# Kernel tuning notes

Hardware: AMD Instinct MI355X
Metric: run time of the kernel (lower is better)

## Reference

```python
import jax, jax.numpy as jnp
import numpy as np

N, E, D = 20000, 640000, 64
NEG_SLOPE = 0.2

def setup_inputs() -> dict:
    key = jax.random.key(0)
    ks = jax.random.split(key, 8)
    x = jax.random.normal(ks[0], (N, D), dtype=jnp.float32)
    edge_index = jax.random.randint(ks[1], (2, E), 0, N, dtype=jnp.int64)
    w0 = jax.random.normal(ks[2], (N, D, D), dtype=jnp.float32) * 0.1
    att0 = jax.random.normal(ks[3], (N, 2 * D, 1), dtype=jnp.float32) * 0.1
    b0 = jax.random.normal(ks[4], (D,), dtype=jnp.float32) * 0.1
    w1 = jax.random.normal(ks[5], (N, D, D), dtype=jnp.float32) * 0.1
    att1 = jax.random.normal(ks[6], (N, 2 * D, 1), dtype=jnp.float32) * 0.1
    b1 = jax.random.normal(ks[7], (D,), dtype=jnp.float32) * 0.1
    return {"x": x, "edge_index": edge_index, "w0": w0, "att0": att0,
            "b0": b0, "w1": w1, "att1": att1, "b1": b1}

def _gat_layer(x, row, col, w, att_w, b):
    n = x.shape[0]
    # per-node dynamic weight bmm: [N,1,D] @ [N,D,D] -> [N,D]
    h = jnp.einsum('nd,nde->ne', x, w)
    h_i = h[row]                      # source messages [E, D]
    h_j = h[col]                      # destination features [E, D]
    att_in = jnp.concatenate([h_i, h_j], axis=1)      # [E, 2D]
    a = att_w[row][:, :, 0]                            # [E, 2D]
    scores = jnp.einsum('ed,ed->e', att_in, a)         # [E]
    scores = jnp.where(scores >= 0, scores, NEG_SLOPE * scores)  # leaky_relu(0.2)
    # segment softmax over destination node (col), replaces python loop over unique(col)
    seg_max = jax.ops.segment_max(scores, col, num_segments=n)
    ex = jnp.exp(scores - seg_max[col])
    seg_sum = jax.ops.segment_sum(ex, col, num_segments=n)
    att = ex / seg_sum[col]
    out = jax.ops.segment_sum(h_i * att[:, None], col, num_segments=n)
    return out + b

def reference(x, edge_index, w0, att0, b0, w1, att1, b1):
    row, col = edge_index[0], edge_index[1]
    h = _gat_layer(x, row, col, w0, att0, b0)
    h = jax.nn.relu(h)  # inter-layer activation; dropout inactive in eval mode
    out = _gat_layer(h, row, col, w1, att1, b1)
    return out
```

## Files before the change

### kernel.cpp

```cpp
#include <hip/hip_runtime.h>
#include <hip/hip_bf16.h>

#define NN 20000
#define EE 640000
#define DD 64


__global__ void zero_kernel(int* __restrict__ p, int n) {
    int i = blockIdx.x * blockDim.x + threadIdx.x;
    if (i < n) p[i] = 0;
}

__global__ void hist_kernel(const int* __restrict__ col, int* __restrict__ counts) {
    int e = blockIdx.x * blockDim.x + threadIdx.x;
    if (e < EE) {
        int c = col[e];
        if ((unsigned)c >= NN) c = 0;
        atomicAdd(&counts[c], 1);
    }
}

__global__ void scan_kernel(const int* __restrict__ counts, int* __restrict__ offsets) {
    const int T = 1024;
    const int per = (NN + T - 1) / T;
    int tid = threadIdx.x;
    int start = tid * per;
    int s = 0;
    for (int i = 0; i < per; ++i) { int idx = start + i; if (idx < NN) s += counts[idx]; }
    __shared__ int sm[T];
    sm[tid] = s;
    __syncthreads();
    for (int off = 1; off < T; off <<= 1) {
        int t = (tid >= off) ? sm[tid - off] : 0;
        __syncthreads();
        sm[tid] += t;
        __syncthreads();
    }
    int run = sm[tid] - s;
    for (int i = 0; i < per; ++i) {
        int idx = start + i;
        if (idx < NN) { offsets[idx] = run; run += counts[idx]; }
    }
    if (tid == T - 1) offsets[NN] = sm[T - 1];
}

__global__ void scatter_kernel(const int* __restrict__ row, const int* __restrict__ col,
                               const int* __restrict__ offsets, int* __restrict__ cursor,
                               int* __restrict__ srcs) {
    int e = blockIdx.x * blockDim.x + threadIdx.x;
    if (e < EE) {
        int c = col[e];
        if ((unsigned)c >= NN) c = 0;
        int r = row[e];
        if ((unsigned)r >= NN) r = 0;
        int p = atomicAdd(&cursor[c], 1);
        srcs[offsets[c] + p] = r;
    }
}


__global__ __launch_bounds__(256) void node_h_kernel(
    const float* __restrict__ x,
    const float* __restrict__ w,
    const float* __restrict__ att,
    float* __restrict__ hs,
    float* __restrict__ s1)
{
    int wave = (blockIdx.x * blockDim.x + threadIdx.x) >> 6;
    int lane = threadIdx.x & 63;
    if (wave >= NN) return;
    int n = wave;

    float xval = x[(size_t)n * 64 + lane];

    int eg = lane & 15;
    int dg = lane >> 4;
    float acc[4] = {0.f, 0.f, 0.f, 0.f};

    const float* wbase = w + (size_t)n * 4096;
    #pragma unroll
    for (int it = 0; it < 16; ++it) {
        int d = it * 4 + dg;
        float xv = __shfl(xval, d, 64);
        float4 r = *(const float4*)(wbase + d * 64 + eg * 4);
        acc[0] += xv * r.x;
        acc[1] += xv * r.y;
        acc[2] += xv * r.z;
        acc[3] += xv * r.w;
    }
    #pragma unroll
    for (int j = 0; j < 4; ++j) {
        acc[j] += __shfl_xor(acc[j], 16, 64);
        acc[j] += __shfl_xor(acc[j], 32, 64);
    }
    if (dg == 0) {
        *(float4*)(hs + (size_t)n * 128 + eg * 4) = make_float4(acc[0], acc[1], acc[2], acc[3]);
    }
    hs[(size_t)n * 128 + 64 + lane] = att[(size_t)n * 128 + 64 + lane];

    float4 a = *(const float4*)(att + (size_t)n * 128 + eg * 4);
    float p = acc[0] * a.x + acc[1] * a.y + acc[2] * a.z + acc[3] * a.w;
    p += __shfl_xor(p, 1, 64);
    p += __shfl_xor(p, 2, 64);
    p += __shfl_xor(p, 4, 64);
    p += __shfl_xor(p, 8, 64);
    if (lane == 0) s1[n] = p;
}


template<bool LAYER0>
__global__ __launch_bounds__(256) void edge_aggr_kernel(
    const float* __restrict__ hs,
    const float* __restrict__ s1,
    const float* __restrict__ bias,
    const int* __restrict__ offsets,
    const int* __restrict__ srcs,
    float* __restrict__ out)
{
    int wave = (blockIdx.x * blockDim.x + threadIdx.x) >> 6;
    int lane = threadIdx.x & 63;
    if (wave >= NN) return;
    int c = wave;

    float hc = hs[(size_t)c * 128 + lane];
    int beg = offsets[c];
    int end = offsets[c + 1];

    float sum0 = 0.f, sum1 = 0.f, sum2 = 0.f, sum3 = 0.f;
    float acc0 = 0.f, acc1 = 0.f, acc2 = 0.f, acc3 = 0.f;

    int i = beg;
    for (; i + 4 <= end; i += 4) {
        int r0 = srcs[i + 0]; if ((unsigned)r0 >= NN) r0 = 0;
        int r1 = srcs[i + 1]; if ((unsigned)r1 >= NN) r1 = 0;
        int r2 = srcs[i + 2]; if ((unsigned)r2 >= NN) r2 = 0;
        int r3 = srcs[i + 3]; if ((unsigned)r3 >= NN) r3 = 0;
        const float* b0p = hs + (size_t)r0 * 128;
        const float* b1p = hs + (size_t)r1 * 128;
        const float* b2p = hs + (size_t)r2 * 128;
        const float* b3p = hs + (size_t)r3 * 128;
        float a20 = b0p[64 + lane];
        float a21 = b1p[64 + lane];
        float a22 = b2p[64 + lane];
        float a23 = b3p[64 + lane];
        float h0 = b0p[lane];
        float h1 = b1p[lane];
        float h2 = b2p[lane];
        float h3 = b3p[lane];
        float s10 = s1[r0], s11 = s1[r1], s12 = s1[r2], s13 = s1[r3];

        float p0 = hc * a20, p1 = hc * a21, p2 = hc * a22, p3 = hc * a23;
        #pragma unroll
        for (int s = 1; s < 64; s <<= 1) {
            p0 += __shfl_xor(p0, s, 64);
            p1 += __shfl_xor(p1, s, 64);
            p2 += __shfl_xor(p2, s, 64);
            p3 += __shfl_xor(p3, s, 64);
        }
        float sc0 = p0 + s10; sc0 = (sc0 >= 0.f) ? sc0 : 0.2f * sc0;
        float sc1 = p1 + s11; sc1 = (sc1 >= 0.f) ? sc1 : 0.2f * sc1;
        float sc2 = p2 + s12; sc2 = (sc2 >= 0.f) ? sc2 : 0.2f * sc2;
        float sc3 = p3 + s13; sc3 = (sc3 >= 0.f) ? sc3 : 0.2f * sc3;
        float e0 = __expf(sc0), e1 = __expf(sc1), e2 = __expf(sc2), e3 = __expf(sc3);
        sum0 += e0; sum1 += e1; sum2 += e2; sum3 += e3;
        acc0 = fmaf(e0, h0, acc0);
        acc1 = fmaf(e1, h1, acc1);
        acc2 = fmaf(e2, h2, acc2);
        acc3 = fmaf(e3, h3, acc3);
    }
    for (; i < end; ++i) {
        int r = srcs[i]; if ((unsigned)r >= NN) r = 0;
        const float* bp = hs + (size_t)r * 128;
        float a2 = bp[64 + lane];
        float hr = bp[lane];
        float p = hc * a2;
        #pragma unroll
        for (int s = 1; s < 64; s <<= 1) p += __shfl_xor(p, s, 64);
        float sc = p + s1[r];
        sc = (sc >= 0.f) ? sc : 0.2f * sc;
        float e = __expf(sc);
        sum0 += e;
        acc0 = fmaf(e, hr, acc0);
    }

    float sum = (sum0 + sum1) + (sum2 + sum3);
    float acc = (acc0 + acc1) + (acc2 + acc3);

    float b = bias[lane];
    float o = (end > beg) ? (acc / sum + b) : b;
    if (LAYER0) o = fmaxf(o, 0.f);
    out[(size_t)c * 64 + lane] = o;
}


extern "C" void kernel_launch(void* const* d_in, const int* in_sizes, int n_in,
                              void* d_out, int out_size, void* d_ws, size_t ws_size,
                              hipStream_t stream) {
    const float* x    = (const float*)d_in[0];
    const int*   ei   = (const int*)d_in[1];
    const float* w0   = (const float*)d_in[2];
    const float* att0 = (const float*)d_in[3];
    const float* b0   = (const float*)d_in[4];
    const float* w1   = (const float*)d_in[5];
    const float* att1 = (const float*)d_in[6];
    const float* b1   = (const float*)d_in[7];

    const int* row = ei;
    const int* col = ei + EE;

    char* base = (char*)d_ws;
    float* hs      = (float*)(base);
    float* xmid    = (float*)(base + 10240000);
    float* s1      = (float*)(base + 15360000);
    int*   counts  = (int*)(base + 15440000);
    int*   cursor  = (int*)(base + 15520000);
    int*   offsets = (int*)(base + 15600000);
    int*   srcs    = (int*)(base + 15680016);

    zero_kernel<<<(2 * NN + 255) / 256, 256, 0, stream>>>(counts, 2 * NN);
    hist_kernel<<<(EE + 255) / 256, 256, 0, stream>>>(col, counts);
    scan_kernel<<<1, 1024, 0, stream>>>(counts, offsets);
    scatter_kernel<<<(EE + 255) / 256, 256, 0, stream>>>(row, col, offsets, cursor, srcs);

    const int hblocks = (NN + 3) / 4;

    node_h_kernel<<<hblocks, 256, 0, stream>>>(x, w0, att0, hs, s1);
    edge_aggr_kernel<true><<<hblocks, 256, 0, stream>>>(hs, s1, b0, offsets, srcs, xmid);
    node_h_kernel<<<hblocks, 256, 0, stream>>>(xmid, w1, att1, hs, s1);
    edge_aggr_kernel<false><<<hblocks, 256, 0, stream>>>(hs, s1, b1, offsets, srcs,
                                                         (float*)d_out);
}
```

Measured before the change: 833.3 us.

## Split wave into four 16-lane groups processing edges with float4 loads

Result: faster. 800.5 us (-3.9%).

```diff
diff --git a/kernel.cpp b/kernel.cpp
--- a/kernel.cpp
+++ b/kernel.cpp
@@ -121,75 +121,95 @@
     int lane = threadIdx.x & 63;
     if (wave >= NN) return;
     int c = wave;
-
-    float hc = hs[(size_t)c * 128 + lane];
+    int g = lane >> 4;
+    int q = lane & 15;
+
+    float4 hcv = *(const float4*)(hs + (size_t)c * 128 + q * 4);
     int beg = offsets[c];
     int end = offsets[c + 1];
 
-    float sum0 = 0.f, sum1 = 0.f, sum2 = 0.f, sum3 = 0.f;
-    float acc0 = 0.f, acc1 = 0.f, acc2 = 0.f, acc3 = 0.f;
-
-    int i = beg;
-    for (; i + 4 <= end; i += 4) {
-        int r0 = srcs[i + 0]; if ((unsigned)r0 >= NN) r0 = 0;
-        int r1 = srcs[i + 1]; if ((unsigned)r1 >= NN) r1 = 0;
-        int r2 = srcs[i + 2]; if ((unsigned)r2 >= NN) r2 = 0;
-        int r3 = srcs[i + 3]; if ((unsigned)r3 >= NN) r3 = 0;
-        const float* b0p = hs + (size_t)r0 * 128;
-        const float* b1p = hs + (size_t)r1 * 128;
-        const float* b2p = hs + (size_t)r2 * 128;
-        const float* b3p = hs + (size_t)r3 * 128;
-        float a20 = b0p[64 + lane];
-        float a21 = b1p[64 + lane];
-        float a22 = b2p[64 + lane];
-        float a23 = b3p[64 + lane];
-        float h0 = b0p[lane];
-        float h1 = b1p[lane];
-        float h2 = b2p[lane];
-        float h3 = b3p[lane];
-        float s10 = s1[r0], s11 = s1[r1], s12 = s1[r2], s13 = s1[r3];
-
-        float p0 = hc * a20, p1 = hc * a21, p2 = hc * a22, p3 = hc * a23;
-        #pragma unroll
-        for (int s = 1; s < 64; s <<= 1) {
-            p0 += __shfl_xor(p0, s, 64);
-            p1 += __shfl_xor(p1, s, 64);
-            p2 += __shfl_xor(p2, s, 64);
-            p3 += __shfl_xor(p3, s, 64);
+    float4 acc0 = make_float4(0.f, 0.f, 0.f, 0.f);
+    float4 acc1 = make_float4(0.f, 0.f, 0.f, 0.f);
+    float sum0 = 0.f, sum1 = 0.f;
+
+    for (int ib = beg; ib < end; ib += 8) {
+        int i0 = ib + g;
+        int i1 = ib + 4 + g;
+        bool v0 = i0 < end;
+        bool v1 = i1 < end;
+        int r0 = 0, r1 = 0;
+        if (v0) { r0 = srcs[i0]; if ((unsigned)r0 >= NN) r0 = 0; }
+        if (v1) { r1 = srcs[i1]; if ((unsigned)r1 >= NN) r1 = 0; }
+        const float* p0 = hs + (size_t)r0 * 128;
+        const float* p1 = hs + (size_t)r1 * 128;
+        float4 a0 = *(const float4*)(p0 + 64 + q * 4);
+        float4 a1 = *(const float4*)(p1 + 64 + q * 4);
+        float4 h0 = *(const float4*)(p0 + q * 4);
+        float4 h1 = *(const float4*)(p1 + q * 4);
+        float t0 = s1[r0];
+        float t1 = s1[r1];
+
+        float d0 = hcv.x * a0.x;
+        d0 = fmaf(hcv.y, a0.y, d0);
+        d0 = fmaf(hcv.z, a0.z, d0);
+        d0 = fmaf(hcv.w, a0.w, d0);
+        float d1 = hcv.x * a1.x;
+        d1 = fmaf(hcv.y, a1.y, d1);
+        d1 = fmaf(hcv.z, a1.z, d1);
+        d1 = fmaf(hcv.w, a1.w, d1);
+        d0 += __shfl_xor(d0, 1, 64);  d1 += __shfl_xor(d1, 1, 64);
+        d0 += __shfl_xor(d0, 2, 64);  d1 += __shfl_xor(d1, 2, 64);
+        d0 += __shfl_xor(d0, 4, 64);  d1 += __shfl_xor(d1, 4, 64);
+        d0 += __shfl_xor(d0, 8, 64);  d1 += __shfl_xor(d1, 8, 64);
+
+        float sc0 = d0 + t0; sc0 = (sc0 >= 0.f) ? sc0 : 0.2f * sc0;
+        float sc1 = d1 + t1; sc1 = (sc1 >= 0.f) ? sc1 : 0.2f * sc1;
+        float e0 = v0 ? __expf(sc0) : 0.f;
+        float e1 = v1 ? __expf(sc1) : 0.f;
+        sum0 += e0;
+        sum1 += e1;
+        acc0.x = fmaf(e0, h0.x, acc0.x);
+        acc0.y = fmaf(e0, h0.y, acc0.y);
+        acc0.z = fmaf(e0, h0.z, acc0.z);
+        acc0.w = fmaf(e0, h0.w, acc0.w);
+        acc1.x = fmaf(e1, h1.x, acc1.x);
+        acc1.y = fmaf(e1, h1.y, acc1.y);
+        acc1.z = fmaf(e1, h1.z, acc1.z);
+        acc1.w = fmaf(e1, h1.w, acc1.w);
+    }
+
+    float sum = sum0 + sum1;
+    float4 acc;
+    acc.x = acc0.x + acc1.x;
+    acc.y = acc0.y + acc1.y;
+    acc.z = acc0.z + acc1.z;
+    acc.w = acc0.w + acc1.w;
+
+    sum   += __shfl_xor(sum,   16, 64);  sum   += __shfl_xor(sum,   32, 64);
+    acc.x += __shfl_xor(acc.x, 16, 64);  acc.x += __shfl_xor(acc.x, 32, 64);
+    acc.y += __shfl_xor(acc.y, 16, 64);  acc.y += __shfl_xor(acc.y, 32, 64);
+    acc.z += __shfl_xor(acc.z, 16, 64);  acc.z += __shfl_xor(acc.z, 32, 64);
+    acc.w += __shfl_xor(acc.w, 16, 64);  acc.w += __shfl_xor(acc.w, 32, 64);
+
+    if (g == 0) {
+        float4 b4 = *(const float4*)(bias + q * 4);
+        float4 o;
+        if (end > beg) {
+            o.x = acc.x / sum + b4.x;
+            o.y = acc.y / sum + b4.y;
+            o.z = acc.z / sum + b4.z;
+            o.w = acc.w / sum + b4.w;
+        } else {
+            o = b4;
         }
-        float sc0 = p0 + s10; sc0 = (sc0 >= 0.f) ? sc0 : 0.2f * sc0;
-        float sc1 = p1 + s11; sc1 = (sc1 >= 0.f) ? sc1 : 0.2f * sc1;
-        float sc2 = p2 + s12; sc2 = (sc2 >= 0.f) ? sc2 : 0.2f * sc2;
-        float sc3 = p3 + s13; sc3 = (sc3 >= 0.f) ? sc3 : 0.2f * sc3;
-        float e0 = __expf(sc0), e1 = __expf(sc1), e2 = __expf(sc2), e3 = __expf(sc3);
-        sum0 += e0; sum1 += e1; sum2 += e2; sum3 += e3;
-        acc0 = fmaf(e0, h0, acc0);
-        acc1 = fmaf(e1, h1, acc1);
-        acc2 = fmaf(e2, h2, acc2);
-        acc3 = fmaf(e3, h3, acc3);
-    }
-    for (; i < end; ++i) {
-        int r = srcs[i]; if ((unsigned)r >= NN) r = 0;
-        const float* bp = hs + (size_t)r * 128;
-        float a2 = bp[64 + lane];
-        float hr = bp[lane];
-        float p = hc * a2;
-        #pragma unroll
-        for (int s = 1; s < 64; s <<= 1) p += __shfl_xor(p, s, 64);
-        float sc = p + s1[r];
-        sc = (sc >= 0.f) ? sc : 0.2f * sc;
-        float e = __expf(sc);
-        sum0 += e;
-        acc0 = fmaf(e, hr, acc0);
-    }
-
-    float sum = (sum0 + sum1) + (sum2 + sum3);
-    float acc = (acc0 + acc1) + (acc2 + acc3);
-
-    float b = bias[lane];
-    float o = (end > beg) ? (acc / sum + b) : b;
-    if (LAYER0) o = fmaxf(o, 0.f);
-    out[(size_t)c * 64 + lane] = o;
+        if (LAYER0) {
+            o.x = fmaxf(o.x, 0.f);
+            o.y = fmaxf(o.y, 0.f);
+            o.z = fmaxf(o.z, 0.f);
+            o.w = fmaxf(o.w, 0.f);
+        }
+        *(float4*)(out + (size_t)c * 64 + q * 4) = o;
+    }
 }
 
 
```
